# Performance work log

Measured on AMD Instinct MI355X. Metric: run time of the kernel, lower is better.

## Reference

```python
import jax, jax.numpy as jnp
import numpy as np

B, S, D = 2, 2048, 2048
QC, KVC = 16, 4          # query heads, kv heads (GQA)
HD = D // QC             # head_dim = 128
FF = 8192                # ff_dim = 4 * model_dim
EPS = 1e-5


def rotate_every_two(x):
    x1 = x[..., ::2]
    x2 = x[..., 1::2]
    return jnp.stack((-x2, x1), axis=-1).reshape(*x.shape[:-1], -1)


def apply_rope(x, seq_len, sin, cos):
    sin = sin[:seq_len]
    cos = cos[:seq_len]
    return x * cos + rotate_every_two(x) * sin


def rmsnorm(x, w, eps=EPS):
    xf = x.astype(jnp.float32)
    xf = xf * jax.lax.rsqrt(jnp.square(xf).mean(-1, keepdims=True) + eps)
    return xf.astype(x.dtype) * w


def attention(x, mask, sin, cos, wqkv, wo):
    b, s, d = x.shape
    kv_repeat = QC // KVC
    qkv = x @ wqkv
    q = qkv[..., :D].reshape(b, s, kv_repeat, KVC, HD)
    q = jnp.moveaxis(q, 1, 3)                       # (b, rep, kvc, s, hd)
    q = apply_rope(q, s, sin, cos)
    k, v = jnp.split(qkv[..., D:], 2, axis=-1)
    k = k.reshape(b, s, KVC, HD).swapaxes(1, 2)     # (b, kvc, s, hd)
    v = v.reshape(b, s, KVC, HD).swapaxes(1, 2)
    k = apply_rope(k, s, sin, cos) * (HD ** -0.5)
    k = k[:, None]                                  # (b, 1, kvc, s, hd)
    v = v[:, None]
    a = q @ k.swapaxes(-2, -1)                      # (b, rep, kvc, s, s)
    a = a + mask[:s, :s]
    a = jax.nn.softmax(a, axis=-1)
    o = a @ v                                       # (b, rep, kvc, s, hd)
    o = o.reshape(b, QC, s, HD).swapaxes(1, 2).reshape(b, s, d)
    return o @ wo


def ffn(x, wk, wv):
    k = jnp.square(jax.nn.relu(x @ wk))
    return k @ wv


def setup_inputs() -> dict:
    key = jax.random.key(0)
    ks = jax.random.split(key, 6)
    std = 0.02
    x = jax.random.normal(ks[0], (B, S, D), jnp.float32)
    wqkv = std * jax.random.normal(ks[1], (D, D + 2 * KVC * HD), jnp.float32)
    wo = std * jax.random.normal(ks[2], (D, D), jnp.float32)
    ffn_wk = std * jax.random.normal(ks[3], (D, FF), jnp.float32)
    ffn_wv = std * jax.random.normal(ks[4], (FF, D), jnp.float32)
    norm1_w = jnp.ones((D,), jnp.float32)
    norm2_w = jnp.ones((D,), jnp.float32)
    # GPT-J style interleaved RoPE tables of shape (S, HD)
    pos = jnp.arange(S, dtype=jnp.float32)
    inv_freq = 1.0 / (10000.0 ** (jnp.arange(0, HD, 2, dtype=jnp.float32) / HD))
    freqs = pos[:, None] * inv_freq[None, :]
    rope_sin = jnp.repeat(jnp.sin(freqs), 2, axis=-1)
    rope_cos = jnp.repeat(jnp.cos(freqs), 2, axis=-1)
    # additive causal mask
    mask = jnp.where(jnp.tril(jnp.ones((S, S), bool)), 0.0, -1e9).astype(jnp.float32)
    return dict(x=x, mask=mask, rope_sin=rope_sin, rope_cos=rope_cos,
                wqkv=wqkv, wo=wo, norm1_w=norm1_w, norm2_w=norm2_w,
                ffn_wk=ffn_wk, ffn_wv=ffn_wv)


def reference(x, mask, rope_sin, rope_cos, wqkv, wo, norm1_w, norm2_w, ffn_wk, ffn_wv):
    # pre-norm residual block
    x = x + attention(rmsnorm(x, norm1_w), mask, rope_sin, rope_cos, wqkv, wo)
    x = x + ffn(rmsnorm(x, norm2_w), ffn_wk, ffn_wv)
    return x
```

## Files before the change

kernel.cpp:

```cpp
#include <hip/hip_runtime.h>
#include <hip/hip_bf16.h>
#include <cstdint>
#include <cstddef>
#include <type_traits>

typedef __hip_bfloat16 bf16;
typedef float f32x4 __attribute__((ext_vector_type(4)));
typedef short s16x8 __attribute__((ext_vector_type(8)));

#define BB 2
#define SS 2048
#define DD 2048
#define QCH 16
#define KVH 4
#define HD 128
#define FF 8192

__device__ __forceinline__ float b2f(bf16 v) { return __bfloat162float(v); }
__device__ __forceinline__ bf16 f2b(float v) { return __float2bfloat16(v); }

__device__ __forceinline__ void gl_lds16(const void* g, void* l) {
    __builtin_amdgcn_global_load_lds((const __attribute__((address_space(1))) void*)g,
                                     (__attribute__((address_space(3))) void*)l,
                                     16, 0, 0);
}

__global__ __launch_bounds__(256) void transpose_cast(const float* __restrict__ src,
                                                      bf16* __restrict__ dst,
                                                      int K, int N) {
    __shared__ float t[32][33];
    int n0 = blockIdx.x * 32, k0 = blockIdx.y * 32;
    int tx = threadIdx.x, ty = threadIdx.y;
#pragma unroll
    for (int j = 0; j < 4; ++j)
        t[ty + j * 8][tx] = src[(size_t)(k0 + ty + j * 8) * N + n0 + tx];
    __syncthreads();
#pragma unroll
    for (int j = 0; j < 4; ++j)
        dst[(size_t)(n0 + ty + j * 8) * K + k0 + tx] = f2b(t[tx][ty + j * 8]);
}

__global__ __launch_bounds__(256) void rmsnorm_k(const float* __restrict__ x,
                                                 const float* __restrict__ w,
                                                 bf16* __restrict__ out) {
    int row = blockIdx.x;
    int tid = threadIdx.x;
    const float* xr = x + (size_t)row * DD + tid * 8;
    f32x4 a0 = *(const f32x4*)xr;
    f32x4 a1 = *(const f32x4*)(xr + 4);
    float f[8];
    float ss = 0.f;
#pragma unroll
    for (int i = 0; i < 4; ++i) { f[i] = a0[i]; f[i + 4] = a1[i]; }
#pragma unroll
    for (int i = 0; i < 8; ++i) ss += f[i] * f[i];
#pragma unroll
    for (int off = 32; off > 0; off >>= 1) ss += __shfl_down(ss, off);
    __shared__ float red[4];
    int lane = tid & 63, wv_ = tid >> 6;
    if (lane == 0) red[wv_] = ss;
    __syncthreads();
    float tot = red[0] + red[1] + red[2] + red[3];
    float scale = rsqrtf(tot * (1.0f / DD) + 1e-5f);
#pragma unroll
    for (int i = 0; i < 8; ++i) {
        int col = tid * 8 + i;
        out[(size_t)row * DD + col] = f2b(f[i] * scale * w[col]);
    }
}

__global__ __launch_bounds__(256) void rope_scatter(const bf16* __restrict__ qkv,
                                                    const float* __restrict__ rsin,
                                                    const float* __restrict__ rcos,
                                                    bf16* __restrict__ q_r,
                                                    bf16* __restrict__ k_r,
                                                    bf16* __restrict__ v_t) {
    int p = blockIdx.x * 256 + threadIdx.x;
    int row = p / 1536;
    int c2 = p - row * 1536;
    int col = c2 * 2;
    int b = row >> 11, s = row & 2047;
    size_t qbase = (size_t)row * 3072 + col;
    float e = b2f(qkv[qbase]);
    float o = b2f(qkv[qbase + 1]);
    if (col < 2048) {
        int h = col >> 7, hd = col & 127;
        float cs = rcos[s * HD + hd];
        float sn = rsin[s * HD + hd];
        size_t base = (((size_t)(b * QCH + h)) * SS + s) * HD + hd;
        q_r[base]     = f2b(e * cs - o * sn);
        q_r[base + 1] = f2b(o * cs + e * sn);
    } else if (col < 2560) {
        int cc = col - 2048;
        int kc = cc >> 7, hd = cc & 127;
        float cs = rcos[s * HD + hd];
        float sn = rsin[s * HD + hd];
        const float kscale = 0.08838834764831845f;
        size_t base = (((size_t)(b * KVH + kc)) * SS + s) * HD + hd;
        k_r[base]     = f2b((e * cs - o * sn) * kscale);
        k_r[base + 1] = f2b((o * cs + e * sn) * kscale);
    } else {
        int cc = col - 2560;
        int kc = cc >> 7, hd = cc & 127;
        size_t base = (((size_t)(b * KVH + kc)) * HD + hd) * SS + s;
        v_t[base]      = qkv[qbase];
        v_t[base + SS] = qkv[qbase + 1];
    }
}

template <int EPI, typename CT>
__global__ __launch_bounds__(256) void gemm_bt(const bf16* __restrict__ A,
                                               const bf16* __restrict__ Bt,
                                               const float* __restrict__ res,
                                               CT* __restrict__ C,
                                               int M, int N, int K) {
    __shared__ __align__(16) bf16 As[2][128 * 32];
    __shared__ __align__(16) bf16 Bs[2][128 * 32];
    const int tid = threadIdx.x;
    const int m0 = blockIdx.y * 128, n0 = blockIdx.x * 128;
    const int lane = tid & 63, w = tid >> 6;
    const int wm = (w >> 1) * 64, wn = (w & 1) * 64;
    const int lm = lane & 15, quad = lane >> 4;

    const int fo = tid * 16;
    const int row0 = tid >> 2;
    const int cb0 = (((tid & 3) ^ ((tid >> 3) & 3)) * 16);

    const char* Ab0 = (const char*)A + (size_t)(m0 + row0) * K * 2 + cb0;
    const char* Ab1 = (const char*)A + (size_t)(m0 + row0 + 64) * K * 2 + cb0;
    const char* Bb0 = (const char*)Bt + (size_t)(n0 + row0) * K * 2 + cb0;
    const char* Bb1 = (const char*)Bt + (size_t)(n0 + row0 + 64) * K * 2 + cb0;

    f32x4 acc[4][4];
    const f32x4 zero = {0.f, 0.f, 0.f, 0.f};
#pragma unroll
    for (int i = 0; i < 4; ++i)
#pragma unroll
        for (int j = 0; j < 4; ++j) acc[i][j] = zero;

    const int NT = K >> 5;
    {
        gl_lds16(Ab0, (char*)&As[0][0] + fo);
        gl_lds16(Ab1, (char*)&As[0][0] + fo + 4096);
        gl_lds16(Bb0, (char*)&Bs[0][0] + fo);
        gl_lds16(Bb1, (char*)&Bs[0][0] + fo + 4096);
    }
    const int sw = (quad ^ ((lm >> 1) & 3)) * 8;

    for (int kt = 0; kt < NT; ++kt) {
        const int cur = kt & 1;
        __syncthreads();
        if (kt + 1 < NT) {
            const int kb = (kt + 1) * 64;
            gl_lds16(Ab0 + kb, (char*)&As[cur ^ 1][0] + fo);
            gl_lds16(Ab1 + kb, (char*)&As[cur ^ 1][0] + fo + 4096);
            gl_lds16(Bb0 + kb, (char*)&Bs[cur ^ 1][0] + fo);
            gl_lds16(Bb1 + kb, (char*)&Bs[cur ^ 1][0] + fo + 4096);
        }
        s16x8 af[4], bfr[4];
#pragma unroll
        for (int mi = 0; mi < 4; ++mi)
            af[mi] = *(const s16x8*)&As[cur][(wm + mi * 16 + lm) * 32 + sw];
#pragma unroll
        for (int ni = 0; ni < 4; ++ni)
            bfr[ni] = *(const s16x8*)&Bs[cur][(wn + ni * 16 + lm) * 32 + sw];
#pragma unroll
        for (int mi = 0; mi < 4; ++mi)
#pragma unroll
            for (int ni = 0; ni < 4; ++ni)
                acc[mi][ni] = __builtin_amdgcn_mfma_f32_16x16x32_bf16(af[mi], bfr[ni], acc[mi][ni], 0, 0, 0);
    }

#pragma unroll
    for (int mi = 0; mi < 4; ++mi)
#pragma unroll
        for (int ni = 0; ni < 4; ++ni) {
            int gr = m0 + wm + mi * 16 + quad * 4;
            int gc = n0 + wn + ni * 16 + lm;
#pragma unroll
            for (int r = 0; r < 4; ++r) {
                size_t idx = (size_t)(gr + r) * N + gc;
                float v = acc[mi][ni][r];
                if (EPI == 1) v += res[idx];
                if (EPI == 2) { v = fmaxf(v, 0.f); v = v * v; }
                if constexpr (std::is_same<CT, float>::value) C[idx] = v;
                else C[idx] = f2b(v);
            }
        }
}

__global__ __launch_bounds__(256) void attn_k(const bf16* __restrict__ q_r,
                                              const bf16* __restrict__ k_r,
                                              const bf16* __restrict__ v_t,
                                              bf16* __restrict__ o_buf) {
    __shared__ __align__(16) bf16 Ks[64 * 128];
    __shared__ __align__(16) bf16 Vs[128 * 64];
    __shared__ __align__(16) bf16 Ps[4][32 * 72];
    const int i = blockIdx.x;
    const int qt = i >> 5, hb = i & 31;
    const int h = hb & 15, b = hb >> 4;
    const int tid = threadIdx.x, w = tid >> 6, lane = tid & 63;
    const int lm = lane & 15, quad = lane >> 4;
    const int kvh = h & (KVH - 1);
    const int qw0 = qt * 128 + w * 32;
    bf16* Pw = &Ps[w][0];

    s16x8 aq[2][4];
#pragma unroll
    for (int mt = 0; mt < 2; ++mt) {
        const bf16* qp = q_r + (((size_t)(b * QCH + h)) * SS + qw0 + mt * 16 + lm) * HD + quad * 8;
#pragma unroll
        for (int c = 0; c < 4; ++c) aq[mt][c] = *(const s16x8*)(qp + c * 32);
    }

    const char* kbase = (const char*)(k_r + ((size_t)(b * KVH + kvh)) * SS * HD);
    const char* vbase = (const char*)(v_t + ((size_t)(b * KVH + kvh)) * HD * SS);

    const int krow = tid >> 4, kslot = tid & 15;
    const int ksrc_off = ((kslot ^ (krow & 15)) * 16);
    const int vrow = tid >> 3, vslot = tid & 7;

    const f32x4 zero = {0.f, 0.f, 0.f, 0.f};
    f32x4 accO[2][8];
#pragma unroll
    for (int mt = 0; mt < 2; ++mt)
#pragma unroll
        for (int ni = 0; ni < 8; ++ni) accO[mt][ni] = zero;
    float lp[2][4] = {{0.f, 0.f, 0.f, 0.f}, {0.f, 0.f, 0.f, 0.f}};

    const int ntiles = 2 * qt + 2;
    for (int kt = 0; kt < ntiles; ++kt) {
        const int kb = kt * 64;
#pragma unroll
        for (int j = 0; j < 4; ++j) {
            int kr = krow + j * 16;
            gl_lds16(kbase + (size_t)(kb + kr) * 256 + ksrc_off, (char*)Ks + tid * 16 + j * 4096);
        }
#pragma unroll
        for (int j = 0; j < 4; ++j) {
            int vr = vrow + j * 32;
            gl_lds16(vbase + (size_t)vr * (SS * 2) + kb * 2 + ((vslot ^ (vr & 7)) * 16),
                     (char*)Vs + tid * 16 + j * 4096);
        }
        __syncthreads();

        const bool active = (kb <= qw0 + 31);
        if (active) {
#pragma unroll
            for (int nt = 0; nt < 4; ++nt) {
                const int krl = nt * 16 + lm;
                s16x8 kf[4];
#pragma unroll
                for (int c = 0; c < 4; ++c)
                    kf[c] = *(const s16x8*)((char*)Ks + krl * 256 + (((c * 4 + quad) ^ lm) * 16));
                const int colk = kb + krl;
#pragma unroll
                for (int mt = 0; mt < 2; ++mt) {
                    f32x4 sc = zero;
#pragma unroll
                    for (int c = 0; c < 4; ++c)
                        sc = __builtin_amdgcn_mfma_f32_16x16x32_bf16(aq[mt][c], kf[c], sc, 0, 0, 0);
#pragma unroll
                    for (int r = 0; r < 4; ++r) {
                        int rowq = qw0 + mt * 16 + quad * 4 + r;
                        float p = (colk <= rowq) ? __expf(sc[r]) : 0.f;
                        lp[mt][r] += p;
                        Pw[(mt * 16 + quad * 4 + r) * 72 + nt * 16 + lm] = f2b(p);
                    }
                }
            }
            s16x8 pf[2][2];
#pragma unroll
            for (int mt = 0; mt < 2; ++mt)
#pragma unroll
                for (int kf2 = 0; kf2 < 2; ++kf2)
                    pf[mt][kf2] = *(const s16x8*)&Pw[(mt * 16 + lm) * 72 + kf2 * 32 + quad * 8];
#pragma unroll
            for (int ni = 0; ni < 8; ++ni) {
                const int vrl = ni * 16 + lm;
#pragma unroll
                for (int kf2 = 0; kf2 < 2; ++kf2) {
                    s16x8 vf = *(const s16x8*)((char*)Vs + vrl * 128 + (((kf2 * 4 + quad) ^ (lm & 7)) * 16));
#pragma unroll
                    for (int mt = 0; mt < 2; ++mt)
                        accO[mt][ni] = __builtin_amdgcn_mfma_f32_16x16x32_bf16(pf[mt][kf2], vf, accO[mt][ni], 0, 0, 0);
                }
            }
        }
        __syncthreads();
    }

#pragma unroll
    for (int mt = 0; mt < 2; ++mt)
#pragma unroll
        for (int r = 0; r < 4; ++r) {
            float l = lp[mt][r];
#pragma unroll
            for (int off = 1; off < 16; off <<= 1) l += __shfl_xor(l, off);
            lp[mt][r] = 1.f / l;
        }

#pragma unroll
    for (int mt = 0; mt < 2; ++mt)
#pragma unroll
        for (int ni = 0; ni < 8; ++ni)
#pragma unroll
            for (int r = 0; r < 4; ++r) {
                int s = qw0 + mt * 16 + quad * 4 + r;
                size_t idx = ((size_t)(b * SS + s)) * DD + h * HD + ni * 16 + lm;
                o_buf[idx] = f2b(accO[mt][ni][r] * lp[mt][r]);
            }
}

extern "C" void kernel_launch(void* const* d_in, const int* in_sizes, int n_in,
                              void* d_out, int out_size, void* d_ws, size_t ws_size,
                              hipStream_t stream) {
    const float* x    = (const float*)d_in[0];
    const float* rsin = (const float*)d_in[2];
    const float* rcos = (const float*)d_in[3];
    const float* wqkv = (const float*)d_in[4];
    const float* wo   = (const float*)d_in[5];
    const float* n1w  = (const float*)d_in[6];
    const float* n2w  = (const float*)d_in[7];
    const float* wk   = (const float*)d_in[8];
    const float* wv   = (const float*)d_in[9];
    float* out = (float*)d_out;

    char* ws = (char*)d_ws;
    size_t off = 0;
    auto allocb = [&](size_t elems) { bf16* p = (bf16*)(ws + off); off += elems * 2; return p; };
    auto allocf = [&](size_t elems) { float* p = (float*)(ws + off); off += elems * 4; return p; };
    bf16* wqkvT = allocb((size_t)3072 * 2048);
    bf16* woT   = allocb((size_t)2048 * 2048);
    bf16* wkT   = allocb((size_t)8192 * 2048);
    bf16* wvT   = allocb((size_t)2048 * 8192);
    bf16* xn    = allocb((size_t)4096 * 2048);
    bf16* qkv   = allocb((size_t)4096 * 3072);
    bf16* q_r   = allocb((size_t)BB * QCH * SS * HD);
    bf16* k_r   = allocb((size_t)BB * KVH * SS * HD);
    bf16* v_t   = allocb((size_t)BB * KVH * HD * SS);
    bf16* ffnh  = allocb((size_t)4096 * 8192);
    float* x1   = allocf((size_t)4096 * 2048);

    dim3 tb(32, 8);
    transpose_cast<<<dim3(3072 / 32, 2048 / 32), tb, 0, stream>>>(wqkv, wqkvT, 2048, 3072);
    transpose_cast<<<dim3(2048 / 32, 2048 / 32), tb, 0, stream>>>(wo, woT, 2048, 2048);
    transpose_cast<<<dim3(8192 / 32, 2048 / 32), tb, 0, stream>>>(wk, wkT, 2048, 8192);
    transpose_cast<<<dim3(2048 / 32, 8192 / 32), tb, 0, stream>>>(wv, wvT, 8192, 2048);

    rmsnorm_k<<<4096, 256, 0, stream>>>(x, n1w, xn);
    gemm_bt<0, bf16><<<dim3(3072 / 128, 4096 / 128), 256, 0, stream>>>(xn, wqkvT, nullptr, qkv, 4096, 3072, 2048);
    rope_scatter<<<(4096 * 1536) / 256, 256, 0, stream>>>(qkv, rsin, rcos, q_r, k_r, v_t);
    attn_k<<<512, 256, 0, stream>>>(q_r, k_r, v_t, qkv );
    gemm_bt<1, float><<<dim3(2048 / 128, 4096 / 128), 256, 0, stream>>>(qkv, woT, x, x1, 4096, 2048, 2048);
    rmsnorm_k<<<4096, 256, 0, stream>>>(x1, n2w, xn);
    gemm_bt<2, bf16><<<dim3(8192 / 128, 4096 / 128), 256, 0, stream>>>(xn, wkT, nullptr, ffnh, 4096, 8192, 2048);
    gemm_bt<1, float><<<dim3(2048 / 128, 4096 / 128), 256, 0, stream>>>(ffnh, wvT, x1, out, 4096, 2048, 8192);
}
```

Before: 862.9 us.

## Replace 128x128 GEMM with 256-wide, 8-wave ping-pong pipelined GEMM kernel

Swaps the simple double-buffered 128x128 bf16 MFMA GEMM for a 512-thread kernel using 256x256 or 128x256 tiles with BK=64. It interleaves LDS fragment loads, global-to-LDS prefetches and MFMA clusters under explicit barriers, waitcnts and setprio. Block indices are remapped so that neighbouring tiles share operands in cache. The goals are higher arithmetic intensity per LDS byte, better latency hiding and better L2 reuse, at the cost of larger register and LDS footprint and a fragile hand-tuned schedule.

```diff
diff --git a/kernel.cpp b/kernel.cpp
--- a/kernel.cpp
+++ b/kernel.cpp
@@ -24,6 +24,9 @@
                                      (__attribute__((address_space(3))) void*)l,
                                      16, 0, 0);
 }
+
+#define GBAR __builtin_amdgcn_s_barrier()
+#define LGK0 do { asm volatile("s_waitcnt lgkmcnt(0)" ::: "memory"); __builtin_amdgcn_sched_barrier(0); } while (0)
 
 __global__ __launch_bounds__(256) void transpose_cast(const float* __restrict__ src,
                                                       bf16* __restrict__ dst,
@@ -108,75 +111,153 @@
     }
 }
 
-template <int EPI, typename CT>
-__global__ __launch_bounds__(256) void gemm_bt(const bf16* __restrict__ A,
-                                               const bf16* __restrict__ Bt,
-                                               const float* __restrict__ res,
-                                               CT* __restrict__ C,
-                                               int M, int N, int K) {
-    __shared__ __align__(16) bf16 As[2][128 * 32];
-    __shared__ __align__(16) bf16 Bs[2][128 * 32];
+template <int MREP, int EPI, typename CT>
+__global__ __launch_bounds__(512, 2) void gemm256(const bf16* __restrict__ A,
+                                                  const bf16* __restrict__ Bt,
+                                                  const float* __restrict__ res,
+                                                  CT* __restrict__ C,
+                                                  int M, int N, int K) {
+    static_assert(MREP == 4 || MREP == 8, "MREP");
+    constexpr int MH  = MREP / 2;
+    constexpr int NJA = MREP / 4;
+    constexpr int BM  = MREP * 32;
+
+    __shared__ __align__(16) bf16 As[2][2][MREP * 1024];
+    __shared__ __align__(16) bf16 Bs[2][2][8192];
+
     const int tid = threadIdx.x;
-    const int m0 = blockIdx.y * 128, n0 = blockIdx.x * 128;
-    const int lane = tid & 63, w = tid >> 6;
-    const int wm = (w >> 1) * 64, wn = (w & 1) * 64;
+    const int w = tid >> 6, lane = tid & 63;
     const int lm = lane & 15, quad = lane >> 4;
-
-    const int fo = tid * 16;
-    const int row0 = tid >> 2;
-    const int cb0 = (((tid & 3) ^ ((tid >> 3) & 3)) * 16);
-
-    const char* Ab0 = (const char*)A + (size_t)(m0 + row0) * K * 2 + cb0;
-    const char* Ab1 = (const char*)A + (size_t)(m0 + row0 + 64) * K * 2 + cb0;
-    const char* Bb0 = (const char*)Bt + (size_t)(n0 + row0) * K * 2 + cb0;
-    const char* Bb1 = (const char*)Bt + (size_t)(n0 + row0 + 64) * K * 2 + cb0;
-
-    f32x4 acc[4][4];
+    const int wm = w >> 2, wn = w & 3;
+
+    const int cpx = gridDim.x >> 3;
+    const int sb = (blockIdx.x & 7) * cpx + (blockIdx.x >> 3);
+    const int nbx = N >> 8;
+    const int bx = sb % nbx, by = sb / nbx;
+    const int m0 = by * BM, n0 = bx * 256;
+
+    const size_t K2 = (size_t)K * 2;
+    const int srow = tid >> 3;
+    const int sboff = ((tid & 7) ^ (srow & 7)) * 16;
+    const int NT = K >> 6;
+
+    const char* Abase = (const char*)A + (size_t)m0 * K2 + sboff;
+    const char* Bbase = (const char*)Bt + (size_t)n0 * K2 + sboff;
+    char* lAs = (char*)&As[0][0][0];
+    char* lBs = (char*)&Bs[0][0][0];
+    constexpr int ASZ = MREP * 2048;
+
+    auto stA = [&](int db, int h, int t) {
+#pragma unroll
+        for (int j = 0; j < NJA; ++j) {
+            int row = h * (MREP * 16) + j * 64 + srow;
+            gl_lds16(Abase + (size_t)row * K2 + (size_t)t * 128,
+                     lAs + (db * 2 + h) * ASZ + j * 8192 + tid * 16);
+        }
+    };
+    auto stB = [&](int db, int h, int t) {
+#pragma unroll
+        for (int j = 0; j < 2; ++j) {
+            int row = h * 128 + j * 64 + srow;
+            gl_lds16(Bbase + (size_t)row * K2 + (size_t)t * 128,
+                     lBs + (db * 2 + h) * 16384 + j * 8192 + tid * 16);
+        }
+    };
+
+    const int c0 = (quad ^ (lm & 7)) * 16;
+    const int c1 = ((4 + quad) ^ (lm & 7)) * 16;
+
+    s16x8 a0[MH][2], a1[MH][2], b0[2][2], b1[2][2];
+    f32x4 acc[MREP][4];
     const f32x4 zero = {0.f, 0.f, 0.f, 0.f};
 #pragma unroll
-    for (int i = 0; i < 4; ++i)
+    for (int i = 0; i < MREP; ++i)
 #pragma unroll
         for (int j = 0; j < 4; ++j) acc[i][j] = zero;
 
-    const int NT = K >> 5;
-    {
-        gl_lds16(Ab0, (char*)&As[0][0] + fo);
-        gl_lds16(Ab1, (char*)&As[0][0] + fo + 4096);
-        gl_lds16(Bb0, (char*)&Bs[0][0] + fo);
-        gl_lds16(Bb1, (char*)&Bs[0][0] + fo + 4096);
+    auto ldA = [&](s16x8 (&a)[MH][2], int db, int mh) {
+        const char* base = lAs + (db * 2 + wm) * ASZ + (mh * (MH * 16) + lm) * 128;
+#pragma unroll
+        for (int mi = 0; mi < MH; ++mi) {
+            a[mi][0] = *(const s16x8*)(base + mi * 2048 + c0);
+            a[mi][1] = *(const s16x8*)(base + mi * 2048 + c1);
+        }
+    };
+    auto ldB = [&](s16x8 (&b)[2][2], int db, int nh) {
+        const char* base = lBs + (db * 2 + (wn >> 1)) * 16384 + ((wn & 1) * 64 + nh * 32 + lm) * 128;
+#pragma unroll
+        for (int ni = 0; ni < 2; ++ni) {
+            b[ni][0] = *(const s16x8*)(base + ni * 2048 + c0);
+            b[ni][1] = *(const s16x8*)(base + ni * 2048 + c1);
+        }
+    };
+    auto mm = [&](s16x8 (&a)[MH][2], s16x8 (&b)[2][2], int mh, int nh) {
+#pragma unroll
+        for (int mi = 0; mi < MH; ++mi)
+#pragma unroll
+            for (int ni = 0; ni < 2; ++ni)
+#pragma unroll
+                for (int kk = 0; kk < 2; ++kk)
+                    acc[mh * MH + mi][nh * 2 + ni] = __builtin_amdgcn_mfma_f32_16x16x32_bf16(
+                        a[mi][kk], b[ni][kk], acc[mh * MH + mi][nh * 2 + ni], 0, 0, 0);
+    };
+
+    stA(0, 0, 0); stA(0, 1, 0); stB(0, 0, 0); stB(0, 1, 0);
+    stA(1, 0, 1); stA(1, 1, 1);
+    if constexpr (NJA == 2) asm volatile("s_waitcnt vmcnt(4)" ::: "memory");
+    else                    asm volatile("s_waitcnt vmcnt(2)" ::: "memory");
+    GBAR;
+
+    const int NI = NT >> 1;
+#pragma unroll 1
+    for (int i = 0; i < NI; ++i) {
+        const int t1 = 2 * i + 1;
+        int tA = 2 * i + 2; if (tA >= NT) tA = 0;
+        int tB = 2 * i + 3; if (tB >= NT) tB = 0;
+        ldA(a0, 0, 0); ldB(b0, 0, 0); stB(1, 0, t1);
+        GBAR; LGK0;
+        __builtin_amdgcn_s_setprio(1); mm(a0, b0, 0, 0); __builtin_amdgcn_s_setprio(0);
+        GBAR;
+        ldA(a1, 0, 1); ldB(b1, 0, 1); stB(1, 1, t1);
+        GBAR; LGK0;
+        __builtin_amdgcn_s_setprio(1); mm(a1, b1, 1, 1); __builtin_amdgcn_s_setprio(0);
+        GBAR;
+        stA(0, 0, tA);
+        GBAR; LGK0;
+        __builtin_amdgcn_s_setprio(1); mm(a0, b1, 0, 1); __builtin_amdgcn_s_setprio(0);
+        GBAR;
+        stA(0, 1, tA);
+        GBAR; LGK0;
+        __builtin_amdgcn_s_setprio(1); mm(a1, b0, 1, 0); __builtin_amdgcn_s_setprio(0);
+        if constexpr (NJA == 2) asm volatile("s_waitcnt vmcnt(4)" ::: "memory");
+        else                    asm volatile("s_waitcnt vmcnt(2)" ::: "memory");
+        GBAR;
+        ldA(a0, 1, 0); ldB(b0, 1, 0); stB(0, 0, tA);
+        GBAR; LGK0;
+        __builtin_amdgcn_s_setprio(1); mm(a0, b0, 0, 0); __builtin_amdgcn_s_setprio(0);
+        GBAR;
+        ldA(a1, 1, 1); ldB(b1, 1, 1); stB(0, 1, tA);
+        GBAR; LGK0;
+        __builtin_amdgcn_s_setprio(1); mm(a1, b1, 1, 1); __builtin_amdgcn_s_setprio(0);
+        GBAR;
+        stA(1, 0, tB);
+        GBAR; LGK0;
+        __builtin_amdgcn_s_setprio(1); mm(a0, b1, 0, 1); __builtin_amdgcn_s_setprio(0);
+        GBAR;
+        stA(1, 1, tB);
+        GBAR; LGK0;
+        __builtin_amdgcn_s_setprio(1); mm(a1, b0, 1, 0); __builtin_amdgcn_s_setprio(0);
+        if constexpr (NJA == 2) asm volatile("s_waitcnt vmcnt(4)" ::: "memory");
+        else                    asm volatile("s_waitcnt vmcnt(2)" ::: "memory");
+        GBAR;
     }
-    const int sw = (quad ^ ((lm >> 1) & 3)) * 8;
-
-    for (int kt = 0; kt < NT; ++kt) {
-        const int cur = kt & 1;
-        __syncthreads();
-        if (kt + 1 < NT) {
-            const int kb = (kt + 1) * 64;
-            gl_lds16(Ab0 + kb, (char*)&As[cur ^ 1][0] + fo);
-            gl_lds16(Ab1 + kb, (char*)&As[cur ^ 1][0] + fo + 4096);
-            gl_lds16(Bb0 + kb, (char*)&Bs[cur ^ 1][0] + fo);
-            gl_lds16(Bb1 + kb, (char*)&Bs[cur ^ 1][0] + fo + 4096);
-        }
-        s16x8 af[4], bfr[4];
-#pragma unroll
-        for (int mi = 0; mi < 4; ++mi)
-            af[mi] = *(const s16x8*)&As[cur][(wm + mi * 16 + lm) * 32 + sw];
-#pragma unroll
-        for (int ni = 0; ni < 4; ++ni)
-            bfr[ni] = *(const s16x8*)&Bs[cur][(wn + ni * 16 + lm) * 32 + sw];
-#pragma unroll
-        for (int mi = 0; mi < 4; ++mi)
-#pragma unroll
-            for (int ni = 0; ni < 4; ++ni)
-                acc[mi][ni] = __builtin_amdgcn_mfma_f32_16x16x32_bf16(af[mi], bfr[ni], acc[mi][ni], 0, 0, 0);
-    }
-
-#pragma unroll
-    for (int mi = 0; mi < 4; ++mi)
+
+#pragma unroll
+    for (int mi = 0; mi < MREP; ++mi)
 #pragma unroll
         for (int ni = 0; ni < 4; ++ni) {
-            int gr = m0 + wm + mi * 16 + quad * 4;
-            int gc = n0 + wn + ni * 16 + lm;
+            int gr = m0 + wm * (MREP * 16) + mi * 16 + quad * 4;
+            int gc = n0 + wn * 64 + ni * 16 + lm;
 #pragma unroll
             for (int r = 0; r < 4; ++r) {
                 size_t idx = (size_t)(gr + r) * N + gc;
@@ -349,11 +430,11 @@
     transpose_cast<<<dim3(2048 / 32, 8192 / 32), tb, 0, stream>>>(wv, wvT, 8192, 2048);
 
     rmsnorm_k<<<4096, 256, 0, stream>>>(x, n1w, xn);
-    gemm_bt<0, bf16><<<dim3(3072 / 128, 4096 / 128), 256, 0, stream>>>(xn, wqkvT, nullptr, qkv, 4096, 3072, 2048);
+    gemm256<8, 0, bf16><<<192, 512, 0, stream>>>(xn, wqkvT, nullptr, qkv, 4096, 3072, 2048);
     rope_scatter<<<(4096 * 1536) / 256, 256, 0, stream>>>(qkv, rsin, rcos, q_r, k_r, v_t);
     attn_k<<<512, 256, 0, stream>>>(q_r, k_r, v_t, qkv );
-    gemm_bt<1, float><<<dim3(2048 / 128, 4096 / 128), 256, 0, stream>>>(qkv, woT, x, x1, 4096, 2048, 2048);
+    gemm256<4, 1, float><<<256, 512, 0, stream>>>(qkv, woT, x, x1, 4096, 2048, 2048);
     rmsnorm_k<<<4096, 256, 0, stream>>>(x1, n2w, xn);
-    gemm_bt<2, bf16><<<dim3(8192 / 128, 4096 / 128), 256, 0, stream>>>(xn, wkT, nullptr, ffnh, 4096, 8192, 2048);
-    gemm_bt<1, float><<<dim3(2048 / 128, 4096 / 128), 256, 0, stream>>>(ffnh, wvT, x1, out, 4096, 2048, 8192);
-}
+    gemm256<8, 2, bf16><<<512, 512, 0, stream>>>(xn, wkT, nullptr, ffnh, 4096, 8192, 2048);
+    gemm256<4, 1, float><<<256, 512, 0, stream>>>(ffnh, wvT, x1, out, 4096, 2048, 8192);
+}
```

Measured after the change: 883.1 us. +2.3%, slower.
